# Kernel tuning notes

Hardware: AMD Instinct MI355X
Metric: run time of the kernel (lower is better)

The kernel has to match this reference:

```python
import jax, jax.numpy as jnp
import numpy as np

LIMIT = 7.0      # self.m.limit
ACT_ALPHA = 1.702  # self.m.alpha (GLU sigmoid slope)
R = 8
LORA_ALPHA = 16.0
SCALING = LORA_ALPHA / R
E, H, F = 8, 2048, 1024
D = 2 * F
B, S, K = 2, 1024, 4


def setup_inputs() -> dict:
    key = jax.random.key(0)
    ks = jax.random.split(key, 12)
    w = 0.02  # realistic weight scale
    return {
        "hidden_states": jax.random.normal(ks[0], (B, S, H), jnp.float32),
        "routing_weights": jax.random.uniform(ks[1], (B * S, K), jnp.float32),
        "gate_up_proj": jax.random.normal(ks[2], (E, H, D), jnp.float32) * w,
        "gate_up_proj_bias": jax.random.normal(ks[3], (E, D), jnp.float32) * w,
        "down_proj": jax.random.normal(ks[4], (E, F, H), jnp.float32) * w,
        "down_proj_bias": jax.random.normal(ks[5], (E, H), jnp.float32) * w,
        "lora_gate_up_A": jax.random.normal(ks[6], (E, H, R), jnp.float32) * w,
        "lora_gate_up_B": jax.random.normal(ks[7], (E, R, D), jnp.float32) * w,
        "lora_down_A": jax.random.normal(ks[8], (E, F, R), jnp.float32) * w,
        "lora_down_B": jax.random.normal(ks[9], (E, R, H), jnp.float32) * w,
        "router_indices": jax.random.randint(ks[10], (B * S, K), 0, E, jnp.int64),
    }


def reference(hidden_states, routing_weights, gate_up_proj, gate_up_proj_bias,
              down_proj, down_proj_bias, lora_gate_up_A, lora_gate_up_B,
              lora_down_A, lora_down_B, router_indices):
    b, s, h = hidden_states.shape
    x = hidden_states.reshape(-1, h)  # [T,H]
    # Combined per-(expert,token) routing weight: sum over top-k slots that hit expert e.
    onehot = jax.nn.one_hot(router_indices, E, dtype=x.dtype)        # [T,K,E]
    w = jnp.einsum('tke,tk->et', onehot, routing_weights)            # [E,T]
    # gate_up projection with inline LoRA (per expert, all tokens; masked by w later)
    lora1 = jnp.einsum('etr,erd->etd', jnp.einsum('th,ehr->etr', x, lora_gate_up_A), lora_gate_up_B)
    gate_up = jnp.einsum('th,ehd->etd', x, gate_up_proj) + SCALING * lora1 + gate_up_proj_bias[:, None, :]
    gate = jnp.minimum(gate_up[..., ::2], LIMIT)                     # [E,T,F]
    up = jnp.clip(gate_up[..., 1::2], -LIMIT, LIMIT)
    glu = gate * jax.nn.sigmoid(gate * ACT_ALPHA)
    gated = (up + 1.0) * glu                                         # [E,T,F]
    # down projection with inline LoRA
    lora2 = jnp.einsum('etr,erh->eth', jnp.einsum('etf,efr->etr', gated, lora_down_A), lora_down_B)
    out = jnp.einsum('etf,efh->eth', gated, down_proj) + SCALING * lora2 + down_proj_bias[:, None, :]
    # scatter-combine: weight each expert output and sum over experts
    next_states = jnp.einsum('et,eth->th', w, out)                   # [T,H]
    return next_states.reshape(b, s, h)
```

## Files before the change

kernel.cpp:

```cpp
#include <hip/hip_runtime.h>
#include <stdint.h>


typedef short bf16x8 __attribute__((ext_vector_type(8)));
typedef float f32x4 __attribute__((ext_vector_type(4)));

__device__ __forceinline__ short bf16r(float f) {
  uint32_t u = __float_as_uint(f);
  u += 0x7fffu + ((u >> 16) & 1u);
  return (short)(u >> 16);
}

__device__ __forceinline__ float bf16f(short s) {
  uint32_t u = ((uint32_t)(uint16_t)s) << 16;
  return __uint_as_float(u);
}

__device__ __forceinline__ void load_lds16(const void* g, void* l) {
  __builtin_amdgcn_global_load_lds((const __attribute__((address_space(1))) void*)g,
                                   (__attribute__((address_space(3))) void*)l,
                                   16, 0, 0);
}

__global__ void k_route(const int* __restrict__ idx_raw, const float* __restrict__ rw,
                        float* __restrict__ w, int* __restrict__ cnt, int* __restrict__ list,
                        int* __restrict__ tok_nh, int* __restrict__ tok_pair) {
  __shared__ int s_nz;
  const int tid = threadIdx.x;
  if (tid == 0) s_nz = 0;
  __syncthreads();
  int found = 0;
  for (int i = tid; i < 4096; i += 256) found |= idx_raw[2 * i + 1];
  if (found) atomicOr(&s_nz, 1);
  __syncthreads();
  const bool is64 = (s_nz == 0);

  const int t = blockIdx.x * 256 + tid;
  int ek[4]; float rk[4];
#pragma unroll
  for (int k = 0; k < 4; k++) {
    ek[k] = is64 ? idx_raw[2 * (t * 4 + k)] : idx_raw[t * 4 + k];
    rk[k] = rw[t * 4 + k];
  }
  int j = 0;
#pragma unroll
  for (int e = 0; e < 8; e++) {
    float s = 0.f;
#pragma unroll
    for (int k = 0; k < 4; k++) s += (ek[k] == e) ? rk[k] : 0.f;
    w[e * 2048 + t] = s;
    if (s != 0.f) {
      int slot = atomicAdd(&cnt[e], 1);
      list[e * 2048 + slot] = t;
      tok_pair[t * 4 + j] = (e << 16) | slot;
      j++;
    }
  }
  tok_nh[t] = j;
}

__global__ void k_prefix(const int* __restrict__ cnt, int* __restrict__ offs) {
  if (threadIdx.x == 0 && blockIdx.x == 0) {
    int s = 0;
    for (int e = 0; e < 8; e++) { offs[e] = s; s += cnt[e]; }
    offs[8] = s;
  }
}

__global__ void k_wprep(const float* __restrict__ W, const float* __restrict__ A,
                        const float* __restrict__ Bm, short* __restrict__ O,
                        int Kd, int Nd) {
  const int e = blockIdx.z;
  const float* We = W + (size_t)e * Kd * Nd;
  const float* Ae = A + (size_t)e * Kd * 8;
  const float* Be = Bm + (size_t)e * 8 * Nd;
  short* Oe = O + (size_t)e * Kd * Nd;
  __shared__ float tile[32][33];
  __shared__ float As[32][9];
  __shared__ float Bs[8][32];
  const int n0 = blockIdx.x * 32, k0 = blockIdx.y * 32;
  const int tx = threadIdx.x & 31, ty = threadIdx.x >> 5;
#pragma unroll
  for (int i = 0; i < 4; i++)
    tile[ty + 8 * i][tx] = We[(size_t)(k0 + ty + 8 * i) * Nd + n0 + tx];
  {
    int kk = threadIdx.x >> 3, r = threadIdx.x & 7;
    As[kk][r] = Ae[(size_t)(k0 + kk) * 8 + r];
  }
  {
    int rr = threadIdx.x >> 5, nn = threadIdx.x & 31;
    Bs[rr][nn] = Be[(size_t)rr * Nd + n0 + nn];
  }
  __syncthreads();
#pragma unroll
  for (int i = 0; i < 4; i++) {
    int n = ty + 8 * i;
    float v = tile[tx][n];
    float l = 0.f;
#pragma unroll
    for (int r = 0; r < 8; r++) l += As[tx][r] * Bs[r][n];
    Oe[(size_t)(n0 + n) * Kd + k0 + tx] = bf16r(v + 2.0f * l);
  }
}

__global__ void k_xconv(const float* __restrict__ x, short* __restrict__ xb) {
  const int i = (blockIdx.x * 256 + threadIdx.x) * 4;
  float4 v = *(const float4*)(x + i);
  short4 s;
  s.x = bf16r(v.x); s.y = bf16r(v.y); s.z = bf16r(v.z); s.w = bf16r(v.w);
  *(short4*)(xb + i) = s;
}

__global__ __launch_bounds__(256) void k_gemm1(
    const short* __restrict__ Xb, const short* __restrict__ W1T,
    const float* __restrict__ bias1, const int* __restrict__ cnt,
    const int* __restrict__ offs, const int* __restrict__ list,
    short* __restrict__ gated) {
  const int e = blockIdx.z;
  const int M = cnt[e];
  const int m0 = blockIdx.y * 128;
  if (m0 >= M) return;
  const int n0 = blockIdx.x * 128;
  const short* Be = W1T + (size_t)e * 2048 * 2048;
  const int* le = list + e * 2048;
  const int off_e = offs[e];

  __shared__ __align__(16) short sA[128 * 32];
  __shared__ __align__(16) short sB[128 * 32];

  const int tid = threadIdx.x;
  const int r0 = tid >> 2;
  const int kq = (tid & 3) << 3;
  const int t0 = le[min(m0 + r0, M - 1)];
  const int t1 = le[min(m0 + r0 + 64, M - 1)];
  const short* ga0 = Xb + (size_t)t0 * 2048 + kq;
  const short* ga1 = Xb + (size_t)t1 * 2048 + kq;
  const short* gb0 = Be + (size_t)(n0 + r0) * 2048 + kq;
  const short* gb1 = Be + (size_t)(n0 + r0 + 64) * 2048 + kq;
  short* lA0 = sA + tid * 8;
  short* lA1 = sA + 2048 + tid * 8;
  short* lB0 = sB + tid * 8;
  short* lB1 = sB + 2048 + tid * 8;

  const int lane = tid & 63;
  const int wave = tid >> 6;
  const int wm = (wave & 1) * 64;
  const int wn = (wave >> 1) * 64;
  const int lm = lane & 15;
  const int quad = lane >> 4;

  f32x4 acc[4][4];
#pragma unroll
  for (int i = 0; i < 4; i++)
#pragma unroll
    for (int j = 0; j < 4; j++) acc[i][j] = (f32x4){0.f, 0.f, 0.f, 0.f};

  for (int kt = 0; kt < 64; kt++) {
    load_lds16(ga0, lA0);
    load_lds16(ga1, lA1);
    load_lds16(gb0, lB0);
    load_lds16(gb1, lB1);
    ga0 += 32; ga1 += 32; gb0 += 32; gb1 += 32;
    __syncthreads();
    bf16x8 a[4], b[4];
#pragma unroll
    for (int mi = 0; mi < 4; mi++)
      a[mi] = *(const bf16x8*)(sA + (wm + mi * 16 + lm) * 32 + quad * 8);
#pragma unroll
    for (int ni = 0; ni < 4; ni++)
      b[ni] = *(const bf16x8*)(sB + (wn + ni * 16 + lm) * 32 + quad * 8);
#pragma unroll
    for (int mi = 0; mi < 4; mi++)
#pragma unroll
      for (int ni = 0; ni < 4; ni++)
        acc[mi][ni] = __builtin_amdgcn_mfma_f32_16x16x32_bf16(a[mi], b[ni], acc[mi][ni], 0, 0, 0);
    __syncthreads();
  }

  const float* be = bias1 + e * 2048;
#pragma unroll
  for (int mi = 0; mi < 4; mi++) {
    const int rbase = m0 + wm + mi * 16 + quad * 4;
#pragma unroll
    for (int ni = 0; ni < 4; ni++) {
      const int col = n0 + wn + ni * 16 + lm;
      const float bias = be[col];
#pragma unroll
      for (int r = 0; r < 4; r++) {
        const int slot = rbase + r;
        float val = acc[mi][ni][r] + bias;
        float other = __shfl_xor(val, 1);
        if (((lane & 1) == 0) && (slot < M)) {
          float g = fminf(val, 7.f);
          float u = fminf(fmaxf(other, -7.f), 7.f);
          float glu = g / (1.f + __expf(-1.702f * g));
          float gv = (u + 1.f) * glu;
          gated[(size_t)(off_e + slot) * 1024 + (col >> 1)] = bf16r(gv);
        }
      }
    }
  }
}

__global__ __launch_bounds__(256) void k_gemm2(
    const short* __restrict__ gated, const short* __restrict__ W2T,
    const int* __restrict__ cnt, const int* __restrict__ offs,
    short* __restrict__ pairbuf) {
  const int e = blockIdx.z;
  const int M = cnt[e];
  const int m0 = blockIdx.y * 128;
  if (m0 >= M) return;
  const int n0 = blockIdx.x * 128;
  const int off_e = offs[e];
  const short* Ae = gated + (size_t)off_e * 1024;
  const short* Be = W2T + (size_t)e * 2048 * 1024;

  __shared__ __align__(16) short sA[128 * 32];
  __shared__ __align__(16) short sB[128 * 32];

  const int tid = threadIdx.x;
  const int r0 = tid >> 2;
  const int kq = (tid & 3) << 3;
  const short* ga0 = Ae + (size_t)min(m0 + r0, M - 1) * 1024 + kq;
  const short* ga1 = Ae + (size_t)min(m0 + r0 + 64, M - 1) * 1024 + kq;
  const short* gb0 = Be + (size_t)(n0 + r0) * 1024 + kq;
  const short* gb1 = Be + (size_t)(n0 + r0 + 64) * 1024 + kq;
  short* lA0 = sA + tid * 8;
  short* lA1 = sA + 2048 + tid * 8;
  short* lB0 = sB + tid * 8;
  short* lB1 = sB + 2048 + tid * 8;

  const int lane = tid & 63;
  const int wave = tid >> 6;
  const int wm = (wave & 1) * 64;
  const int wn = (wave >> 1) * 64;
  const int lm = lane & 15;
  const int quad = lane >> 4;

  f32x4 acc[4][4];
#pragma unroll
  for (int i = 0; i < 4; i++)
#pragma unroll
    for (int j = 0; j < 4; j++) acc[i][j] = (f32x4){0.f, 0.f, 0.f, 0.f};

  for (int kt = 0; kt < 32; kt++) {
    load_lds16(ga0, lA0);
    load_lds16(ga1, lA1);
    load_lds16(gb0, lB0);
    load_lds16(gb1, lB1);
    ga0 += 32; ga1 += 32; gb0 += 32; gb1 += 32;
    __syncthreads();
    bf16x8 a[4], b[4];
#pragma unroll
    for (int mi = 0; mi < 4; mi++)
      a[mi] = *(const bf16x8*)(sA + (wm + mi * 16 + lm) * 32 + quad * 8);
#pragma unroll
    for (int ni = 0; ni < 4; ni++)
      b[ni] = *(const bf16x8*)(sB + (wn + ni * 16 + lm) * 32 + quad * 8);
#pragma unroll
    for (int mi = 0; mi < 4; mi++)
#pragma unroll
      for (int ni = 0; ni < 4; ni++)
        acc[mi][ni] = __builtin_amdgcn_mfma_f32_16x16x32_bf16(a[mi], b[ni], acc[mi][ni], 0, 0, 0);
    __syncthreads();
  }

#pragma unroll
  for (int mi = 0; mi < 4; mi++) {
#pragma unroll
    for (int r = 0; r < 4; r++) {
      const int slot = m0 + wm + mi * 16 + quad * 4 + r;
      if (slot >= M) continue;
      short* prow = pairbuf + (size_t)(off_e + slot) * 2048;
#pragma unroll
      for (int ni = 0; ni < 4; ni++) {
        const int h = n0 + wn + ni * 16 + lm;
        prow[h] = bf16r(acc[mi][ni][r]);
      }
    }
  }
}

__global__ __launch_bounds__(256) void k_combine(
    const short* __restrict__ pairbuf, const float* __restrict__ bias2,
    const float* __restrict__ wbuf, const int* __restrict__ offs,
    const int* __restrict__ tok_nh, const int* __restrict__ tok_pair,
    float* __restrict__ out) {
  const int t = blockIdx.x;
  const int h0 = threadIdx.x * 8;
  const int nh = tok_nh[t];
  float acc[8];
#pragma unroll
  for (int i = 0; i < 8; i++) acc[i] = 0.f;
  for (int j = 0; j < nh; j++) {
    const int p = tok_pair[t * 4 + j];
    const int e = p >> 16, slot = p & 0xffff;
    const float wt = wbuf[e * 2048 + t];
    const bf16x8 v = *(const bf16x8*)(pairbuf + (size_t)(offs[e] + slot) * 2048 + h0);
    const float4 bA = *(const float4*)(bias2 + e * 2048 + h0);
    const float4 bB = *(const float4*)(bias2 + e * 2048 + h0 + 4);
    acc[0] += wt * (bf16f(v[0]) + bA.x);
    acc[1] += wt * (bf16f(v[1]) + bA.y);
    acc[2] += wt * (bf16f(v[2]) + bA.z);
    acc[3] += wt * (bf16f(v[3]) + bA.w);
    acc[4] += wt * (bf16f(v[4]) + bB.x);
    acc[5] += wt * (bf16f(v[5]) + bB.y);
    acc[6] += wt * (bf16f(v[6]) + bB.z);
    acc[7] += wt * (bf16f(v[7]) + bB.w);
  }
  float4 oA = {acc[0], acc[1], acc[2], acc[3]};
  float4 oB = {acc[4], acc[5], acc[6], acc[7]};
  *(float4*)(out + (size_t)t * 2048 + h0) = oA;
  *(float4*)(out + (size_t)t * 2048 + h0 + 4) = oB;
}

extern "C" void kernel_launch(void* const* d_in, const int* in_sizes, int n_in,
                              void* d_out, int out_size, void* d_ws, size_t ws_size,
                              hipStream_t stream) {
  const float* x   = (const float*)d_in[0];
  const float* rw  = (const float*)d_in[1];
  const float* w1  = (const float*)d_in[2];
  const float* b1  = (const float*)d_in[3];
  const float* w2  = (const float*)d_in[4];
  const float* b2  = (const float*)d_in[5];
  const float* a1  = (const float*)d_in[6];
  const float* lb1 = (const float*)d_in[7];
  const float* a2  = (const float*)d_in[8];
  const float* lb2 = (const float*)d_in[9];
  const int* idx   = (const int*)d_in[10];
  float* out = (float*)d_out;

  char* ws = (char*)d_ws;
  int* cnt     = (int*)(ws);
  int* offs    = (int*)(ws + 64);
  int* tok_nh  = (int*)(ws + 128);
  float* wbuf  = (float*)(ws + 16384);
  int* list    = (int*)(ws + 81920);
  int* tok_pair= (int*)(ws + 147456);
  short* Xb    = (short*)(ws + (1ull << 20));
  short* gated = (short*)(ws + 9437184ull);
  short* W2T   = (short*)(ws + 26214400ull);
  short* W1T   = (short*)(ws + 59768832ull);
  short* pairbuf = (short*)(ws + 59768832ull);

  hipMemsetAsync(cnt, 0, 64, stream);

  k_route<<<dim3(8), dim3(256), 0, stream>>>(idx, rw, wbuf, cnt, list, tok_nh, tok_pair);
  k_prefix<<<dim3(1), dim3(64), 0, stream>>>(cnt, offs);
  k_wprep<<<dim3(64, 64, 8), dim3(256), 0, stream>>>(w1, a1, lb1, W1T, 2048, 2048);
  k_wprep<<<dim3(64, 32, 8), dim3(256), 0, stream>>>(w2, a2, lb2, W2T, 1024, 2048);
  k_xconv<<<dim3(4096), dim3(256), 0, stream>>>(x, Xb);
  k_gemm1<<<dim3(16, 16, 8), dim3(256), 0, stream>>>(Xb, W1T, b1, cnt, offs, list, gated);
  k_gemm2<<<dim3(16, 16, 8), dim3(256), 0, stream>>>(gated, W2T, cnt, offs, pairbuf);
  k_combine<<<dim3(2048), dim3(256), 0, stream>>>(pairbuf, b2, wbuf, offs, tok_nh, tok_pair, out);
}
```

Before: 464.2 us.

## Replace expert GEMMs with 256x256 double-buffered, swizzled, phase-scheduled MFMA kernel

Merges the two grouped GEMM kernels into one templated 512-thread kernel. It uses 256x256 output tiles, a 64-wide K step and double-buffered LDS with XOR-swizzled layout, and overlaps global-to-LDS loads with MFMA phases using explicit barriers, waitcnt and setprio. The goal is higher data reuse per tile, no LDS bank conflicts, and hidden load latency. The weight-prep kernel also processes 64 rows of K per block instead of 32. In exchange the kernel uses 128KB of LDS and large accumulator register sets, which limits occupancy. The larger tiles also waste more work on the partly filled last tile of each expert.

```diff
diff --git a/kernel.cpp b/kernel.cpp
--- a/kernel.cpp
+++ b/kernel.cpp
@@ -75,31 +75,33 @@
   const float* Ae = A + (size_t)e * Kd * 8;
   const float* Be = Bm + (size_t)e * 8 * Nd;
   short* Oe = O + (size_t)e * Kd * Nd;
-  __shared__ float tile[32][33];
-  __shared__ float As[32][9];
+  __shared__ float tile[64][33];
+  __shared__ float As[64][9];
   __shared__ float Bs[8][32];
-  const int n0 = blockIdx.x * 32, k0 = blockIdx.y * 32;
+  const int n0 = blockIdx.x * 32, k0 = blockIdx.y * 64;
   const int tx = threadIdx.x & 31, ty = threadIdx.x >> 5;
 #pragma unroll
-  for (int i = 0; i < 4; i++)
+  for (int i = 0; i < 8; i++)
     tile[ty + 8 * i][tx] = We[(size_t)(k0 + ty + 8 * i) * Nd + n0 + tx];
   {
     int kk = threadIdx.x >> 3, r = threadIdx.x & 7;
     As[kk][r] = Ae[(size_t)(k0 + kk) * 8 + r];
+    As[kk + 32][r] = Ae[(size_t)(k0 + kk + 32) * 8 + r];
   }
   {
     int rr = threadIdx.x >> 5, nn = threadIdx.x & 31;
     Bs[rr][nn] = Be[(size_t)rr * Nd + n0 + nn];
   }
   __syncthreads();
-#pragma unroll
-  for (int i = 0; i < 4; i++) {
-    int n = ty + 8 * i;
-    float v = tile[tx][n];
+  const int kk2 = threadIdx.x & 63, ng = threadIdx.x >> 6;
+#pragma unroll
+  for (int i = 0; i < 8; i++) {
+    int n = ng + 4 * i;
+    float v = tile[kk2][n];
     float l = 0.f;
 #pragma unroll
-    for (int r = 0; r < 8; r++) l += As[tx][r] * Bs[r][n];
-    Oe[(size_t)(n0 + n) * Kd + k0 + tx] = bf16r(v + 2.0f * l);
+    for (int r = 0; r < 8; r++) l += As[kk2][r] * Bs[r][n];
+    Oe[(size_t)(n0 + n) * Kd + k0 + kk2] = bf16r(v + 2.0f * l);
   }
 }
 
@@ -111,171 +113,189 @@
   *(short4*)(xb + i) = s;
 }
 
-__global__ __launch_bounds__(256) void k_gemm1(
-    const short* __restrict__ Xb, const short* __restrict__ W1T,
-    const float* __restrict__ bias1, const int* __restrict__ cnt,
+
+#define PH_SYNC() do { \
+    asm volatile("s_barrier" ::: "memory"); \
+    asm volatile("s_waitcnt lgkmcnt(0)" ::: "memory"); \
+    __builtin_amdgcn_sched_barrier(0); \
+    __builtin_amdgcn_s_setprio(1); } while (0)
+#define PH_END() do { \
+    __builtin_amdgcn_s_setprio(0); \
+    asm volatile("s_barrier" ::: "memory"); } while (0)
+#define PH_END_GATE() do { \
+    __builtin_amdgcn_s_setprio(0); \
+    asm volatile("s_waitcnt vmcnt(4)" ::: "memory"); \
+    asm volatile("s_barrier" ::: "memory"); } while (0)
+
+#define MM(AARR, BARR, MG, NG) \
+  _Pragma("unroll") \
+  for (int f_ = 0; f_ < 4; ++f_) \
+    _Pragma("unroll") \
+    for (int g_ = 0; g_ < 2; ++g_) \
+      _Pragma("unroll") \
+      for (int s_ = 0; s_ < 2; ++s_) \
+        acc[(MG) + f_][(NG) + g_] = __builtin_amdgcn_mfma_f32_16x16x32_bf16( \
+            AARR[f_][s_], BARR[g_][s_], acc[(MG) + f_][(NG) + g_], 0, 0, 0);
+
+template <int KDIM, bool GATHER, bool GLU>
+__global__ __launch_bounds__(512) void k_gemm8p(
+    const short* __restrict__ Abuf, const short* __restrict__ Bbuf,
+    const float* __restrict__ bias, const int* __restrict__ cnt,
     const int* __restrict__ offs, const int* __restrict__ list,
-    short* __restrict__ gated) {
+    short* __restrict__ outbuf) {
+  constexpr int KT = KDIM / 64;
+  constexpr int NIT = KT / 2;
   const int e = blockIdx.z;
   const int M = cnt[e];
-  const int m0 = blockIdx.y * 128;
+  const int m0 = blockIdx.y * 256;
   if (m0 >= M) return;
-  const int n0 = blockIdx.x * 128;
-  const short* Be = W1T + (size_t)e * 2048 * 2048;
-  const int* le = list + e * 2048;
+  const int n0 = blockIdx.x * 256;
   const int off_e = offs[e];
-
-  __shared__ __align__(16) short sA[128 * 32];
-  __shared__ __align__(16) short sB[128 * 32];
+  const short* Bp = Bbuf + (size_t)e * 2048 * KDIM;
+
+  __shared__ __align__(16) short sA[2 * 256 * 64];
+  __shared__ __align__(16) short sB[2 * 256 * 64];
+  constexpr int SLOT = 256 * 64;
+  constexpr int HALF = 128 * 64;
 
   const int tid = threadIdx.x;
-  const int r0 = tid >> 2;
-  const int kq = (tid & 3) << 3;
-  const int t0 = le[min(m0 + r0, M - 1)];
-  const int t1 = le[min(m0 + r0 + 64, M - 1)];
-  const short* ga0 = Xb + (size_t)t0 * 2048 + kq;
-  const short* ga1 = Xb + (size_t)t1 * 2048 + kq;
-  const short* gb0 = Be + (size_t)(n0 + r0) * 2048 + kq;
-  const short* gb1 = Be + (size_t)(n0 + r0 + 64) * 2048 + kq;
-  short* lA0 = sA + tid * 8;
-  short* lA1 = sA + 2048 + tid * 8;
-  short* lB0 = sB + tid * 8;
-  short* lB1 = sB + 2048 + tid * 8;
-
   const int lane = tid & 63;
-  const int wave = tid >> 6;
-  const int wm = (wave & 1) * 64;
-  const int wn = (wave >> 1) * 64;
+  const int wv = tid >> 6;
+  const int wr = wv >> 2;
+  const int wc = wv & 3;
   const int lm = lane & 15;
   const int quad = lane >> 4;
 
-  f32x4 acc[4][4];
-#pragma unroll
-  for (int i = 0; i < 4; i++)
-#pragma unroll
-    for (int j = 0; j < 4; j++) acc[i][j] = (f32x4){0.f, 0.f, 0.f, 0.f};
-
-  for (int kt = 0; kt < 64; kt++) {
-    load_lds16(ga0, lA0);
-    load_lds16(ga1, lA1);
-    load_lds16(gb0, lB0);
-    load_lds16(gb1, lB1);
-    ga0 += 32; ga1 += 32; gb0 += 32; gb1 += 32;
-    __syncthreads();
-    bf16x8 a[4], b[4];
-#pragma unroll
-    for (int mi = 0; mi < 4; mi++)
-      a[mi] = *(const bf16x8*)(sA + (wm + mi * 16 + lm) * 32 + quad * 8);
-#pragma unroll
-    for (int ni = 0; ni < 4; ni++)
-      b[ni] = *(const bf16x8*)(sB + (wn + ni * 16 + lm) * 32 + quad * 8);
-#pragma unroll
-    for (int mi = 0; mi < 4; mi++)
-#pragma unroll
-      for (int ni = 0; ni < 4; ni++)
-        acc[mi][ni] = __builtin_amdgcn_mfma_f32_16x16x32_bf16(a[mi], b[ni], acc[mi][ni], 0, 0, 0);
-    __syncthreads();
-  }
-
-  const float* be = bias1 + e * 2048;
-#pragma unroll
-  for (int mi = 0; mi < 4; mi++) {
-    const int rbase = m0 + wm + mi * 16 + quad * 4;
-#pragma unroll
-    for (int ni = 0; ni < 4; ni++) {
-      const int col = n0 + wn + ni * 16 + lm;
-      const float bias = be[col];
-#pragma unroll
-      for (int r = 0; r < 4; r++) {
-        const int slot = rbase + r;
-        float val = acc[mi][ni][r] + bias;
-        float other = __shfl_xor(val, 1);
-        if (((lane & 1) == 0) && (slot < M)) {
-          float g = fminf(val, 7.f);
-          float u = fminf(fmaxf(other, -7.f), 7.f);
-          float glu = g / (1.f + __expf(-1.702f * g));
-          float gv = (u + 1.f) * glu;
-          gated[(size_t)(off_e + slot) * 1024 + (col >> 1)] = bf16r(gv);
+  const int srow = tid >> 3;
+  const int scol = ((tid & 7) ^ (srow & 7)) * 8;
+  uint32_t offA[4], offB[4];
+#pragma unroll
+  for (int j = 0; j < 4; ++j) {
+    const int r = m0 + srow + 64 * j;
+    const int rc = min(r, M - 1);
+    if constexpr (GATHER) {
+      offA[j] = (uint32_t)list[e * 2048 + rc] * (uint32_t)KDIM + (uint32_t)scol;
+    } else {
+      offA[j] = (uint32_t)(off_e + rc) * (uint32_t)KDIM + (uint32_t)scol;
+    }
+    offB[j] = (uint32_t)(n0 + srow + 64 * j) * (uint32_t)KDIM + (uint32_t)scol;
+  }
+
+  auto stageA = [&](int slot, int h, int kt) {
+    short* d = sA + slot * SLOT + h * HALF + tid * 8;
+    load_lds16(Abuf + offA[2 * h] + kt * 64, d);
+    load_lds16(Abuf + offA[2 * h + 1] + kt * 64, d + 4096);
+  };
+  auto stageB = [&](int slot, int h, int kt) {
+    short* d = sB + slot * SLOT + h * HALF + tid * 8;
+    load_lds16(Bp + offB[2 * h] + kt * 64, d);
+    load_lds16(Bp + offB[2 * h + 1] + kt * 64, d + 4096);
+  };
+
+  const int rbA = (wr * 128 + lm) * 64;
+  const int rbB = (wc * 64 + lm) * 64;
+  const int c0 = ((0 + quad) ^ (lane & 7)) * 8;
+  const int c1 = ((4 + quad) ^ (lane & 7)) * 8;
+
+  auto rdA = [&](int slot, int mg, bf16x8 (&a)[4][2]) {
+#pragma unroll
+    for (int f = 0; f < 4; ++f) {
+      const short* p = sA + slot * SLOT + rbA + (mg + f) * 1024;
+      a[f][0] = *(const bf16x8*)(p + c0);
+      a[f][1] = *(const bf16x8*)(p + c1);
+    }
+  };
+  auto rdB = [&](int slot, int ng, bf16x8 (&b)[2][2]) {
+#pragma unroll
+    for (int g = 0; g < 2; ++g) {
+      const short* p = sB + slot * SLOT + rbB + (ng + g) * 1024;
+      b[g][0] = *(const bf16x8*)(p + c0);
+      b[g][1] = *(const bf16x8*)(p + c1);
+    }
+  };
+
+  f32x4 acc[8][4];
+#pragma unroll
+  for (int i = 0; i < 8; ++i)
+#pragma unroll
+    for (int j = 0; j < 4; ++j) acc[i][j] = (f32x4){0.f, 0.f, 0.f, 0.f};
+
+  stageB(0, 0, 0); stageB(0, 1, 0);
+  stageA(0, 0, 0); stageA(0, 1, 0);
+  {
+    const int k1 = (1 < KT - 1) ? 1 : (KT - 1);
+    stageB(1, 0, k1); stageB(1, 1, k1);
+  }
+  asm volatile("s_waitcnt vmcnt(4)" ::: "memory");
+  asm volatile("s_barrier" ::: "memory");
+
+  bf16x8 aLo[4][2], aHi[4][2], bLo[2][2], bHi[2][2];
+
+#pragma unroll 1
+  for (int it = 0; it < NIT; ++it) {
+    const int tb = 2 * it + 1;
+    const int tS0 = min(2 * it + 2, KT - 1);
+    const int tS1 = min(2 * it + 3, KT - 1);
+    rdA(0, 0, aLo); rdB(0, 0, bLo);
+    stageA(1, 0, tb);
+    PH_SYNC(); MM(aLo, bLo, 0, 0); PH_END();
+    rdB(0, 2, bHi);
+    stageA(1, 1, tb);
+    PH_SYNC(); MM(aLo, bHi, 0, 2); PH_END();
+    rdA(0, 4, aHi);
+    stageB(0, 0, tS0);
+    PH_SYNC(); MM(aHi, bLo, 4, 0); PH_END();
+    stageB(0, 1, tS0);
+    PH_SYNC(); MM(aHi, bHi, 4, 2); PH_END_GATE();
+    rdA(1, 0, aLo); rdB(1, 0, bLo);
+    stageA(0, 0, tS0);
+    PH_SYNC(); MM(aLo, bLo, 0, 0); PH_END();
+    rdB(1, 2, bHi);
+    stageA(0, 1, tS0);
+    PH_SYNC(); MM(aLo, bHi, 0, 2); PH_END();
+    rdA(1, 4, aHi);
+    stageB(1, 0, tS1);
+    PH_SYNC(); MM(aHi, bLo, 4, 0); PH_END();
+    stageB(1, 1, tS1);
+    PH_SYNC(); MM(aHi, bHi, 4, 2); PH_END_GATE();
+  }
+
+  if constexpr (GLU) {
+    const float* be = bias + e * 2048;
+#pragma unroll
+    for (int m = 0; m < 8; ++m) {
+      const int rbase = m0 + wr * 128 + m * 16 + quad * 4;
+#pragma unroll
+      for (int g = 0; g < 4; ++g) {
+        const int col = n0 + wc * 64 + g * 16 + lm;
+        const float bb = be[col];
+#pragma unroll
+        for (int r = 0; r < 4; ++r) {
+          const int slot = rbase + r;
+          float val = acc[m][g][r] + bb;
+          float other = __shfl_xor(val, 1);
+          if (((lane & 1) == 0) && (slot < M)) {
+            float gt = fminf(val, 7.f);
+            float u = fminf(fmaxf(other, -7.f), 7.f);
+            float glu = gt / (1.f + __expf(-1.702f * gt));
+            outbuf[(size_t)(off_e + slot) * 1024 + (col >> 1)] = bf16r((u + 1.f) * glu);
+          }
         }
       }
     }
-  }
-}
-
-__global__ __launch_bounds__(256) void k_gemm2(
-    const short* __restrict__ gated, const short* __restrict__ W2T,
-    const int* __restrict__ cnt, const int* __restrict__ offs,
-    short* __restrict__ pairbuf) {
-  const int e = blockIdx.z;
-  const int M = cnt[e];
-  const int m0 = blockIdx.y * 128;
-  if (m0 >= M) return;
-  const int n0 = blockIdx.x * 128;
-  const int off_e = offs[e];
-  const short* Ae = gated + (size_t)off_e * 1024;
-  const short* Be = W2T + (size_t)e * 2048 * 1024;
-
-  __shared__ __align__(16) short sA[128 * 32];
-  __shared__ __align__(16) short sB[128 * 32];
-
-  const int tid = threadIdx.x;
-  const int r0 = tid >> 2;
-  const int kq = (tid & 3) << 3;
-  const short* ga0 = Ae + (size_t)min(m0 + r0, M - 1) * 1024 + kq;
-  const short* ga1 = Ae + (size_t)min(m0 + r0 + 64, M - 1) * 1024 + kq;
-  const short* gb0 = Be + (size_t)(n0 + r0) * 1024 + kq;
-  const short* gb1 = Be + (size_t)(n0 + r0 + 64) * 1024 + kq;
-  short* lA0 = sA + tid * 8;
-  short* lA1 = sA + 2048 + tid * 8;
-  short* lB0 = sB + tid * 8;
-  short* lB1 = sB + 2048 + tid * 8;
-
-  const int lane = tid & 63;
-  const int wave = tid >> 6;
-  const int wm = (wave & 1) * 64;
-  const int wn = (wave >> 1) * 64;
-  const int lm = lane & 15;
-  const int quad = lane >> 4;
-
-  f32x4 acc[4][4];
-#pragma unroll
-  for (int i = 0; i < 4; i++)
-#pragma unroll
-    for (int j = 0; j < 4; j++) acc[i][j] = (f32x4){0.f, 0.f, 0.f, 0.f};
-
-  for (int kt = 0; kt < 32; kt++) {
-    load_lds16(ga0, lA0);
-    load_lds16(ga1, lA1);
-    load_lds16(gb0, lB0);
-    load_lds16(gb1, lB1);
-    ga0 += 32; ga1 += 32; gb0 += 32; gb1 += 32;
-    __syncthreads();
-    bf16x8 a[4], b[4];
-#pragma unroll
-    for (int mi = 0; mi < 4; mi++)
-      a[mi] = *(const bf16x8*)(sA + (wm + mi * 16 + lm) * 32 + quad * 8);
-#pragma unroll
-    for (int ni = 0; ni < 4; ni++)
-      b[ni] = *(const bf16x8*)(sB + (wn + ni * 16 + lm) * 32 + quad * 8);
-#pragma unroll
-    for (int mi = 0; mi < 4; mi++)
-#pragma unroll
-      for (int ni = 0; ni < 4; ni++)
-        acc[mi][ni] = __builtin_amdgcn_mfma_f32_16x16x32_bf16(a[mi], b[ni], acc[mi][ni], 0, 0, 0);
-    __syncthreads();
-  }
-
-#pragma unroll
-  for (int mi = 0; mi < 4; mi++) {
-#pragma unroll
-    for (int r = 0; r < 4; r++) {
-      const int slot = m0 + wm + mi * 16 + quad * 4 + r;
-      if (slot >= M) continue;
-      short* prow = pairbuf + (size_t)(off_e + slot) * 2048;
-#pragma unroll
-      for (int ni = 0; ni < 4; ni++) {
-        const int h = n0 + wn + ni * 16 + lm;
-        prow[h] = bf16r(acc[mi][ni][r]);
+  } else {
+#pragma unroll
+    for (int m = 0; m < 8; ++m) {
+#pragma unroll
+      for (int r = 0; r < 4; ++r) {
+        const int slot = m0 + wr * 128 + m * 16 + quad * 4 + r;
+        if (slot >= M) continue;
+        short* prow = outbuf + (size_t)(off_e + slot) * 2048;
+#pragma unroll
+        for (int g = 0; g < 4; ++g) {
+          const int h = n0 + wc * 64 + g * 16 + lm;
+          prow[h] = bf16r(acc[m][g][r]);
+        }
       }
     }
   }
@@ -347,10 +367,12 @@
 
   k_route<<<dim3(8), dim3(256), 0, stream>>>(idx, rw, wbuf, cnt, list, tok_nh, tok_pair);
   k_prefix<<<dim3(1), dim3(64), 0, stream>>>(cnt, offs);
-  k_wprep<<<dim3(64, 64, 8), dim3(256), 0, stream>>>(w1, a1, lb1, W1T, 2048, 2048);
-  k_wprep<<<dim3(64, 32, 8), dim3(256), 0, stream>>>(w2, a2, lb2, W2T, 1024, 2048);
+  k_wprep<<<dim3(64, 32, 8), dim3(256), 0, stream>>>(w1, a1, lb1, W1T, 2048, 2048);
+  k_wprep<<<dim3(64, 16, 8), dim3(256), 0, stream>>>(w2, a2, lb2, W2T, 1024, 2048);
   k_xconv<<<dim3(4096), dim3(256), 0, stream>>>(x, Xb);
-  k_gemm1<<<dim3(16, 16, 8), dim3(256), 0, stream>>>(Xb, W1T, b1, cnt, offs, list, gated);
-  k_gemm2<<<dim3(16, 16, 8), dim3(256), 0, stream>>>(gated, W2T, cnt, offs, pairbuf);
+  k_gemm8p<2048, true, true><<<dim3(8, 8, 8), dim3(512), 0, stream>>>(
+      Xb, W1T, b1, cnt, offs, list, gated);
+  k_gemm8p<1024, false, false><<<dim3(8, 8, 8), dim3(512), 0, stream>>>(
+      gated, W2T, nullptr, cnt, offs, nullptr, pairbuf);
   k_combine<<<dim3(2048), dim3(256), 0, stream>>>(pairbuf, b2, wbuf, offs, tok_nh, tok_pair, out);
 }
```

Result: faster. 432.9 us (-6.7%).
